# Optimization experiments

Hardware: AMD Instinct MI355X
Metric: run time of the kernel (lower is better)

The kernel has to match this reference:

```python
import jax, jax.numpy as jnp
import numpy as np

B, N, D, H = 8, 2048, 768, 64

def setup_inputs() -> dict:
    key = jax.random.key(0)
    k1, k2, k3, k4 = jax.random.split(key, 4)
    return {
        "input": jax.random.normal(k1, (B, N, D), dtype=jnp.float32),
        "Wq": jax.random.normal(k2, (D, H), dtype=jnp.float32) * (D ** -0.5),
        "Wk": jax.random.normal(k3, (D, H), dtype=jnp.float32) * (D ** -0.5),
        "Wv": jax.random.normal(k4, (D, H), dtype=jnp.float32) * (D ** -0.5),
    }

def reference(input, Wq, Wk, Wv):
    # Projections: [B, N, H]
    Q = jnp.einsum('bnd,dh->bnh', input, Wq)
    K = jnp.einsum('bnd,dh->bnh', input, Wk)
    V = jnp.einsum('bnd,dh->bnh', input, Wv)
    # Raw scores [B, N, N]; mask BEFORE scaling (as in original; -inf/scale == -inf)
    scores = jnp.einsum('bqh,bkh->bqk', Q, K)
    n = input.shape[1]
    causal = jnp.tril(jnp.ones((n, n), dtype=bool))
    scores = jnp.where(causal, scores, -jnp.inf)
    scores = scores / (K.shape[-1] ** 0.5)
    attn = jax.nn.softmax(scores, axis=-1)
    # dropout_rate=0 -> identity (eval mode)
    return jnp.einsum('bqk,bkh->bqh', attn, V)
```

## Files before the change

### kernel.cpp

```cpp
#include <hip/hip_runtime.h>
#include <stdint.h>

typedef __bf16 bf16_t;
typedef __bf16 bf16x4 __attribute__((ext_vector_type(4)));
typedef __bf16 bf16x8 __attribute__((ext_vector_type(8)));
typedef float floatx4 __attribute__((ext_vector_type(4)));
typedef float floatx16 __attribute__((ext_vector_type(16)));

#define B_ 8
#define N_ 2048
#define D_ 768
#define H_ 64

#define WAIT_VM8()   { __builtin_amdgcn_sched_barrier(0); __builtin_amdgcn_s_waitcnt(0x0F78); __builtin_amdgcn_sched_barrier(0); }
#define WAIT_VM0()   { __builtin_amdgcn_sched_barrier(0); __builtin_amdgcn_s_waitcnt(0x0F70); __builtin_amdgcn_sched_barrier(0); }
#define WAIT_LGKM0() { __builtin_amdgcn_sched_barrier(0); __builtin_amdgcn_s_waitcnt(0xC07F); __builtin_amdgcn_sched_barrier(0); }

__device__ __forceinline__ bf16_t f2bf(float f) {
    union { float f; uint32_t u; } v; v.f = f;
    uint32_t u = v.u;
    uint32_t r = (u + 0x7fffu + ((u >> 16) & 1u)) >> 16;
    union { unsigned short s; bf16_t b; } o; o.s = (unsigned short)r;
    return o.b;
}

__device__ __forceinline__ void async_cp16(void* l, const void* g) {
    __builtin_amdgcn_global_load_lds(
        (const __attribute__((address_space(1))) uint32_t*)g,
        (__attribute__((address_space(3))) uint32_t*)l, 16, 0, 0);
}

__global__ void wt_kernel(const float* __restrict__ Wq,
                          const float* __restrict__ Wk,
                          const float* __restrict__ Wv,
                          bf16_t* __restrict__ Wt) {
    const int h = threadIdx.x;
    const int k = blockIdx.x;
    const int s = blockIdx.y;
    const float* W = (s == 0) ? Wq : (s == 1) ? Wk : Wv;
    float v = W[k * H_ + h];
    if (s == 0) v *= 0.125f * 1.4426950408889634f;
    Wt[(size_t)(s * 64 + h) * D_ + k] = f2bf(v);
}

__launch_bounds__(256, 2)
__global__ void proj_kernel(const float* __restrict__ X,
                            const bf16_t* __restrict__ Wt,
                            bf16_t* __restrict__ Qb,
                            bf16_t* __restrict__ Kb,
                            bf16_t* __restrict__ Vt) {
    const int wave = threadIdx.x >> 6;
    const int lane = threadIdx.x & 63;
    const int quad = lane >> 4;
    const int l16  = lane & 15;
    const int rowhalf = wave & 1;
    const int colhalf = wave >> 1;
    const int m0blk = blockIdx.x * 32;

    __shared__ __align__(16) float  As[2][32 * 64];
    __shared__ __align__(16) bf16_t Bs[2][192 * 64];

    floatx4 acc[6];
#pragma unroll
    for (int i = 0; i < 6; i++) acc[i] = (floatx4){0.f, 0.f, 0.f, 0.f};

    auto stage = [&](int buf, int k0) {
#pragma unroll
        for (int i = 0; i < 2; i++) {
            const int r = (wave * 2 + i) * 4 + (lane >> 4);
            const int c = (lane & 15) ^ (r & 15);
            const float* g = X + (size_t)(m0blk + r) * D_ + k0 + c * 4;
            async_cp16((char*)&As[buf][0] + (wave * 2 + i) * 1024, g);
        }
#pragma unroll
        for (int i = 0; i < 6; i++) {
            const int r = (wave * 6 + i) * 8 + (lane >> 3);
            const int c = (lane & 7) ^ (r & 7);
            const bf16_t* g = Wt + (size_t)r * D_ + k0 + c * 8;
            async_cp16((char*)&Bs[buf][0] + (wave * 6 + i) * 1024, g);
        }
    };

    const int arow = rowhalf * 16 + l16;

    stage(0, 0);
    for (int ch = 0; ch < 12; ch++) {
        __syncthreads();
        if (ch + 1 < 12) stage((ch + 1) & 1, (ch + 1) * 64);

        const char* Ab = (const char*)&As[ch & 1][0];
        const char* Bb = (const char*)&Bs[ch & 1][0];
#pragma unroll
        for (int kh = 0; kh < 2; kh++) {
            const int c0 = kh * 8 + quad * 2;
            float4 xa = *(const float4*)(Ab + arow * 256 + ((c0 ^ l16) & 15) * 16);
            float4 xb = *(const float4*)(Ab + arow * 256 + (((c0 + 1) ^ l16) & 15) * 16);
            bf16x8 af;
            af[0] = f2bf(xa.x); af[1] = f2bf(xa.y);
            af[2] = f2bf(xa.z); af[3] = f2bf(xa.w);
            af[4] = f2bf(xb.x); af[5] = f2bf(xb.y);
            af[6] = f2bf(xb.z); af[7] = f2bf(xb.w);
            const int cb = kh * 4 + quad;
#pragma unroll
            for (int nt = 0; nt < 6; nt++) {
                const int n = colhalf * 96 + nt * 16 + l16;
                bf16x8 bf = *(const bf16x8*)(Bb + n * 128 + ((cb ^ (n & 7))) * 16);
                acc[nt] = __builtin_amdgcn_mfma_f32_16x16x32_bf16(af, bf, acc[nt], 0, 0, 0);
            }
        }
    }

#pragma unroll
    for (int nt = 0; nt < 6; nt++) {
        const int c = colhalf * 96 + nt * 16 + l16;
#pragma unroll
        for (int r = 0; r < 4; r++) {
            const int m = m0blk + rowhalf * 16 + quad * 4 + r;
            bf16_t val = f2bf(acc[nt][r]);
            if (c < 64) {
                Qb[(size_t)m * H_ + c] = val;
            } else if (c < 128) {
                Kb[(size_t)m * H_ + (c - 64)] = val;
            } else {
                const int b = m >> 11, n = m & 2047, h = c - 128;
                Vt[((size_t)b * H_ + h) * N_ + n] = val;
            }
        }
    }
}

__launch_bounds__(256, 2)
__global__ void attn_kernel(const bf16_t* __restrict__ Qb,
                            const bf16_t* __restrict__ Kb,
                            const bf16_t* __restrict__ Vt,
                            float* __restrict__ Out) {
    const int x = blockIdx.x;
    const int b = blockIdx.y;
    const int z = blockIdx.z;
    const int qt = z ? (63 - x) : x;
    const int q0 = qt * 32;

    const int wave = threadIdx.x >> 6;
    const int lane = threadIdx.x & 63;
    const int hi   = lane >> 5;
    const int lq   = lane & 31;

    __shared__ __align__(16) char smem[4 * 16384 + 4 * 2048];
    char* mybase = smem + wave * 16384;
    char* Pimg   = smem + 65536 + wave * 2048;
    float* Ol = (float*)smem;
    float* Ll = (float*)(smem + 24576);

    const bf16_t* qrow = Qb + ((size_t)b * N_ + q0 + lq) * H_ + hi * 8;
    bf16x8 qf0 = *(const bf16x8*)(qrow);
    bf16x8 qf1 = *(const bf16x8*)(qrow + 16);
    bf16x8 qf2 = *(const bf16x8*)(qrow + 32);
    bf16x8 qf3 = *(const bf16x8*)(qrow + 48);

    floatx16 o0, o1;
#pragma unroll
    for (int i = 0; i < 16; i++) { o0[i] = 0.f; o1[i] = 0.f; }
    float ls = 0.f;

    const bf16_t* KpB = Kb + (size_t)b * N_ * H_;
    const bf16_t* VpB = Vt + (size_t)b * H_ * N_;

    const int rK = lane >> 3, cK = lane & 7;
    const int rV = lane >> 2, cV = lane & 3;
    const int mVl = (rV & 3) ^ ((rV & 4) >> 2);
    auto stage_kv = [&](int k0, char* buf) {
#pragma unroll
        for (int i = 0; i < 4; i++) {
            const int r = i * 8 + rK;
            const int mk = rK ^ (((i & 1) << 2));
            async_cp16(buf + i * 1024,
                       KpB + (size_t)(k0 + r) * H_ + (cK ^ mk) * 8);
        }
#pragma unroll
        for (int i = 0; i < 4; i++) {
            const int h = i * 16 + rV;
            async_cp16(buf + 4096 + i * 1024,
                       VpB + (size_t)h * N_ + k0 + (cV ^ mVl) * 8);
        }
    };

    const int ktm = qt;
    if (wave <= ktm)     stage_kv(wave * 32, mybase);
    if (wave + 4 <= ktm) stage_kv((wave + 4) * 32, mybase + 8192);

    const int mK = (lq & 7) ^ ((lq & 8) >> 1);
    const int m8 = (lq & 7) ^ ((lq & 8) >> 1);

    for (int kt = wave; kt <= ktm; kt += 4) {
        const int k0 = kt * 32;
        char* kb = mybase + (((((kt - wave) >> 2) & 1)) ? 8192 : 0);
        char* vb = kb + 4096;

        if (kt + 4 <= ktm) { WAIT_VM8(); } else { WAIT_VM0(); }

        bf16x8 kf0 = *(const bf16x8*)(kb + lq * 128 + (((0 + hi) ^ mK) * 16));
        bf16x8 kf1 = *(const bf16x8*)(kb + lq * 128 + (((2 + hi) ^ mK) * 16));
        bf16x8 kf2 = *(const bf16x8*)(kb + lq * 128 + (((4 + hi) ^ mK) * 16));
        bf16x8 kf3 = *(const bf16x8*)(kb + lq * 128 + (((6 + hi) ^ mK) * 16));
        const int mV0 = (lq & 3) ^ ((lq & 4) >> 2);
        bf16x8 vf00 = *(const bf16x8*)(vb + (lq     ) * 64 + (((0 + hi) ^ mV0) * 16));
        bf16x8 vf01 = *(const bf16x8*)(vb + (lq     ) * 64 + (((2 + hi) ^ mV0) * 16));
        bf16x8 vf10 = *(const bf16x8*)(vb + (lq + 32) * 64 + (((0 + hi) ^ mV0) * 16));
        bf16x8 vf11 = *(const bf16x8*)(vb + (lq + 32) * 64 + (((2 + hi) ^ mV0) * 16));

        WAIT_LGKM0();
        if (kt + 8 <= ktm) stage_kv(k0 + 256, kb);

        floatx16 st;
#pragma unroll
        for (int i = 0; i < 16; i++) st[i] = 0.f;
        st = __builtin_amdgcn_mfma_f32_32x32x16_bf16(kf0, qf0, st, 0, 0, 0);
        st = __builtin_amdgcn_mfma_f32_32x32x16_bf16(kf1, qf1, st, 0, 0, 0);
        st = __builtin_amdgcn_mfma_f32_32x32x16_bf16(kf2, qf2, st, 0, 0, 0);
        st = __builtin_amdgcn_mfma_f32_32x32x16_bf16(kf3, qf3, st, 0, 0, 0);

        float p[16];
        if (kt < qt) {
#pragma unroll
            for (int r = 0; r < 16; r++) p[r] = exp2f(st[r]);
        } else {
#pragma unroll
            for (int r = 0; r < 16; r++) {
                const int row = (r & 3) + 8 * (r >> 2) + 4 * hi;
                p[r] = (row <= lq) ? exp2f(st[r]) : 0.f;
            }
        }
#pragma unroll
        for (int r = 0; r < 16; r++) ls += p[r];

#pragma unroll
        for (int g = 0; g < 4; g++) {
            bf16x4 w;
            w[0] = f2bf(p[g * 4 + 0]); w[1] = f2bf(p[g * 4 + 1]);
            w[2] = f2bf(p[g * 4 + 2]); w[3] = f2bf(p[g * 4 + 3]);
            const int sub = g * 2 + hi;
            *(bf16x4*)(Pimg + lq * 64 + ((sub ^ m8) * 8)) = w;
        }

#pragma unroll
        for (int s2 = 0; s2 < 2; s2++) {
            const int sub0 = s2 * 4 + hi * 2;
            bf16x4 a0 = *(const bf16x4*)(Pimg + lq * 64 + (((sub0    ) ^ m8) * 8));
            bf16x4 a1 = *(const bf16x4*)(Pimg + lq * 64 + (((sub0 + 1) ^ m8) * 8));
            bf16x8 pf;
            pf[0] = a0[0]; pf[1] = a0[1]; pf[2] = a0[2]; pf[3] = a0[3];
            pf[4] = a1[0]; pf[5] = a1[1]; pf[6] = a1[2]; pf[7] = a1[3];
            o0 = __builtin_amdgcn_mfma_f32_32x32x16_bf16(pf, (s2 ? vf01 : vf00), o0, 0, 0, 0);
            o1 = __builtin_amdgcn_mfma_f32_32x32x16_bf16(pf, (s2 ? vf11 : vf10), o1, 0, 0, 0);
        }
    }

    float lst = ls + __shfl_xor(ls, 32, 64);
    __syncthreads();
    if (hi == 0) Ll[wave * 32 + lq] = lst;
    if (wave != 0) {
        float* Ow = Ol + (wave - 1) * 2048;
#pragma unroll
        for (int r = 0; r < 16; r++) {
            const int q = (r & 3) + 8 * (r >> 2) + 4 * hi;
            Ow[q * 64 + lq]      = o0[r];
            Ow[q * 64 + 32 + lq] = o1[r];
        }
    }
    __syncthreads();
    if (wave == 0) {
#pragma unroll
        for (int r = 0; r < 16; r++) {
            const int q = (r & 3) + 8 * (r >> 2) + 4 * hi;
            const float l4 = Ll[q] + Ll[32 + q] + Ll[64 + q] + Ll[96 + q];
            const float inv = 1.0f / l4;
            float v0 = o0[r] + Ol[q * 64 + lq]
                     + Ol[2048 + q * 64 + lq] + Ol[4096 + q * 64 + lq];
            float v1 = o1[r] + Ol[q * 64 + 32 + lq]
                     + Ol[2048 + q * 64 + 32 + lq] + Ol[4096 + q * 64 + 32 + lq];
            const size_t base = ((size_t)b * N_ + q0 + q) * H_;
            Out[base + lq]      = v0 * inv;
            Out[base + 32 + lq] = v1 * inv;
        }
    }
}

extern "C" void kernel_launch(void* const* d_in, const int* in_sizes, int n_in,
                              void* d_out, int out_size, void* d_ws, size_t ws_size,
                              hipStream_t stream) {
    const float* X  = (const float*)d_in[0];
    const float* Wq = (const float*)d_in[1];
    const float* Wk = (const float*)d_in[2];
    const float* Wv = (const float*)d_in[3];
    float* Out = (float*)d_out;

    char* ws = (char*)d_ws;
    bf16_t* Qb = (bf16_t*)(ws);
    bf16_t* Kb = (bf16_t*)(ws + (size_t)(2u << 20));
    bf16_t* Vt = (bf16_t*)(ws + (size_t)(4u << 20));
    bf16_t* Wt = (bf16_t*)(ws + (size_t)(6u << 20));

    hipLaunchKernelGGL(wt_kernel, dim3(768, 3), dim3(64), 0, stream, Wq, Wk, Wv, Wt);
    hipLaunchKernelGGL(proj_kernel, dim3(512), dim3(256), 0, stream, X, Wt, Qb, Kb, Vt);
    hipLaunchKernelGGL(attn_kernel, dim3(32, 8, 2), dim3(256), 0, stream, Qb, Kb, Vt, Out);
}
```

Measured before the change: 120.9 us.

## Split projection columns across blocks and widen attention to eight waves

The projection kernel now splits the 192 output columns across two blocks, which doubles the grid and halves per-block LDS and accumulators. The attention kernel moves to 512 threads with eight waves splitting the key tiles. V is loaded straight from global memory instead of being staged in LDS. The P matrix is repacked into MFMA operand layout with cross-lane shuffles rather than an LDS round trip, and the final reduction is spread over all threads with vectorized stores. These changes aim for more parallelism and less LDS traffic, at the cost of re-reading X twice and issuing uncoalesced, latency-exposed global V loads in the inner loop.

```diff
diff --git a/kernel.cpp b/kernel.cpp
--- a/kernel.cpp
+++ b/kernel.cpp
@@ -2,7 +2,6 @@
 #include <stdint.h>
 
 typedef __bf16 bf16_t;
-typedef __bf16 bf16x4 __attribute__((ext_vector_type(4)));
 typedef __bf16 bf16x8 __attribute__((ext_vector_type(8)));
 typedef float floatx4 __attribute__((ext_vector_type(4)));
 typedef float floatx16 __attribute__((ext_vector_type(16)));
@@ -12,7 +11,6 @@
 #define D_ 768
 #define H_ 64
 
-#define WAIT_VM8()   { __builtin_amdgcn_sched_barrier(0); __builtin_amdgcn_s_waitcnt(0x0F78); __builtin_amdgcn_sched_barrier(0); }
 #define WAIT_VM0()   { __builtin_amdgcn_sched_barrier(0); __builtin_amdgcn_s_waitcnt(0x0F70); __builtin_amdgcn_sched_barrier(0); }
 #define WAIT_LGKM0() { __builtin_amdgcn_sched_barrier(0); __builtin_amdgcn_s_waitcnt(0xC07F); __builtin_amdgcn_sched_barrier(0); }
 
@@ -22,6 +20,12 @@
     uint32_t r = (u + 0x7fffu + ((u >> 16) & 1u)) >> 16;
     union { unsigned short s; bf16_t b; } o; o.s = (unsigned short)r;
     return o.b;
+}
+
+__device__ __forceinline__ uint32_t pkbf(float lo, float hi_) {
+    union { bf16_t b[2]; uint32_t u; } t;
+    t.b[0] = f2bf(lo); t.b[1] = f2bf(hi_);
+    return t.u;
 }
 
 __device__ __forceinline__ void async_cp16(void* l, const void* g) {
@@ -43,7 +47,7 @@
     Wt[(size_t)(s * 64 + h) * D_ + k] = f2bf(v);
 }
 
-__launch_bounds__(256, 2)
+__launch_bounds__(256, 4)
 __global__ void proj_kernel(const float* __restrict__ X,
                             const bf16_t* __restrict__ Wt,
                             bf16_t* __restrict__ Qb,
@@ -55,14 +59,16 @@
     const int l16  = lane & 15;
     const int rowhalf = wave & 1;
     const int colhalf = wave >> 1;
-    const int m0blk = blockIdx.x * 32;
+    const int nb = blockIdx.x & 1;
+    const int colbase = nb * 96;
+    const int m0blk = (blockIdx.x >> 1) * 32;
 
     __shared__ __align__(16) float  As[2][32 * 64];
-    __shared__ __align__(16) bf16_t Bs[2][192 * 64];
-
-    floatx4 acc[6];
-#pragma unroll
-    for (int i = 0; i < 6; i++) acc[i] = (floatx4){0.f, 0.f, 0.f, 0.f};
+    __shared__ __align__(16) bf16_t Bs[2][96 * 64];
+
+    floatx4 acc[3];
+#pragma unroll
+    for (int i = 0; i < 3; i++) acc[i] = (floatx4){0.f, 0.f, 0.f, 0.f};
 
     auto stage = [&](int buf, int k0) {
 #pragma unroll
@@ -73,11 +79,11 @@
             async_cp16((char*)&As[buf][0] + (wave * 2 + i) * 1024, g);
         }
 #pragma unroll
-        for (int i = 0; i < 6; i++) {
-            const int r = (wave * 6 + i) * 8 + (lane >> 3);
+        for (int i = 0; i < 3; i++) {
+            const int r = (wave * 3 + i) * 8 + (lane >> 3);
             const int c = (lane & 7) ^ (r & 7);
-            const bf16_t* g = Wt + (size_t)r * D_ + k0 + c * 8;
-            async_cp16((char*)&Bs[buf][0] + (wave * 6 + i) * 1024, g);
+            const bf16_t* g = Wt + (size_t)(colbase + r) * D_ + k0 + c * 8;
+            async_cp16((char*)&Bs[buf][0] + (wave * 3 + i) * 1024, g);
         }
     };
 
@@ -102,17 +108,17 @@
             af[6] = f2bf(xb.z); af[7] = f2bf(xb.w);
             const int cb = kh * 4 + quad;
 #pragma unroll
-            for (int nt = 0; nt < 6; nt++) {
-                const int n = colhalf * 96 + nt * 16 + l16;
-                bf16x8 bf = *(const bf16x8*)(Bb + n * 128 + ((cb ^ (n & 7))) * 16);
+            for (int nt = 0; nt < 3; nt++) {
+                const int nl = colhalf * 48 + nt * 16 + l16;
+                bf16x8 bf = *(const bf16x8*)(Bb + nl * 128 + ((cb ^ (nl & 7))) * 16);
                 acc[nt] = __builtin_amdgcn_mfma_f32_16x16x32_bf16(af, bf, acc[nt], 0, 0, 0);
             }
         }
     }
 
 #pragma unroll
-    for (int nt = 0; nt < 6; nt++) {
-        const int c = colhalf * 96 + nt * 16 + l16;
+    for (int nt = 0; nt < 3; nt++) {
+        const int c = colbase + colhalf * 48 + nt * 16 + l16;
 #pragma unroll
         for (int r = 0; r < 4; r++) {
             const int m = m0blk + rowhalf * 16 + quad * 4 + r;
@@ -129,7 +135,7 @@
     }
 }
 
-__launch_bounds__(256, 2)
+__launch_bounds__(512, 4)
 __global__ void attn_kernel(const bf16_t* __restrict__ Qb,
                             const bf16_t* __restrict__ Kb,
                             const bf16_t* __restrict__ Vt,
@@ -140,16 +146,19 @@
     const int qt = z ? (63 - x) : x;
     const int q0 = qt * 32;
 
-    const int wave = threadIdx.x >> 6;
-    const int lane = threadIdx.x & 63;
+    const int tid  = threadIdx.x;
+    const int wave = tid >> 6;
+    const int lane = tid & 63;
     const int hi   = lane >> 5;
     const int lq   = lane & 31;
 
-    __shared__ __align__(16) char smem[4 * 16384 + 4 * 2048];
-    char* mybase = smem + wave * 16384;
-    char* Pimg   = smem + 65536 + wave * 2048;
+    __shared__ __align__(16) char smem[8 * 8192 + 1024];
+    char* mybase = smem + wave * 8192;
     float* Ol = (float*)smem;
-    float* Ll = (float*)(smem + 24576);
+    float* Ll = (float*)(smem + 65536);
+
+    const bf16_t* KpB = Kb + (size_t)b * N_ * H_;
+    const bf16_t* VpB = Vt + (size_t)b * H_ * N_;
 
     const bf16_t* qrow = Qb + ((size_t)b * N_ + q0 + lq) * H_ + hi * 8;
     bf16x8 qf0 = *(const bf16x8*)(qrow);
@@ -162,54 +171,43 @@
     for (int i = 0; i < 16; i++) { o0[i] = 0.f; o1[i] = 0.f; }
     float ls = 0.f;
 
-    const bf16_t* KpB = Kb + (size_t)b * N_ * H_;
-    const bf16_t* VpB = Vt + (size_t)b * H_ * N_;
-
     const int rK = lane >> 3, cK = lane & 7;
-    const int rV = lane >> 2, cV = lane & 3;
-    const int mVl = (rV & 3) ^ ((rV & 4) >> 2);
-    auto stage_kv = [&](int k0, char* buf) {
+    auto stage_k = [&](int k0, char* buf) {
 #pragma unroll
         for (int i = 0; i < 4; i++) {
             const int r = i * 8 + rK;
-            const int mk = rK ^ (((i & 1) << 2));
+            const int mk = rK ^ ((i & 1) << 2);
             async_cp16(buf + i * 1024,
                        KpB + (size_t)(k0 + r) * H_ + (cK ^ mk) * 8);
         }
-#pragma unroll
-        for (int i = 0; i < 4; i++) {
-            const int h = i * 16 + rV;
-            async_cp16(buf + 4096 + i * 1024,
-                       VpB + (size_t)h * N_ + k0 + (cV ^ mVl) * 8);
-        }
     };
 
     const int ktm = qt;
-    if (wave <= ktm)     stage_kv(wave * 32, mybase);
-    if (wave + 4 <= ktm) stage_kv((wave + 4) * 32, mybase + 8192);
+    if (wave <= ktm)     stage_k(wave * 32, mybase);
+    if (wave + 8 <= ktm) stage_k((wave + 8) * 32, mybase + 4096);
 
     const int mK = (lq & 7) ^ ((lq & 8) >> 1);
-    const int m8 = (lq & 7) ^ ((lq & 8) >> 1);
-
-    for (int kt = wave; kt <= ktm; kt += 4) {
+
+    for (int kt = wave; kt <= ktm; kt += 8) {
         const int k0 = kt * 32;
-        char* kb = mybase + (((((kt - wave) >> 2) & 1)) ? 8192 : 0);
-        char* vb = kb + 4096;
-
-        if (kt + 4 <= ktm) { WAIT_VM8(); } else { WAIT_VM0(); }
+        char* kb = mybase + (((kt - wave) >> 3) & 1) * 4096;
+
+        if (kt == wave) { WAIT_VM0(); }
 
         bf16x8 kf0 = *(const bf16x8*)(kb + lq * 128 + (((0 + hi) ^ mK) * 16));
         bf16x8 kf1 = *(const bf16x8*)(kb + lq * 128 + (((2 + hi) ^ mK) * 16));
         bf16x8 kf2 = *(const bf16x8*)(kb + lq * 128 + (((4 + hi) ^ mK) * 16));
         bf16x8 kf3 = *(const bf16x8*)(kb + lq * 128 + (((6 + hi) ^ mK) * 16));
-        const int mV0 = (lq & 3) ^ ((lq & 4) >> 2);
-        bf16x8 vf00 = *(const bf16x8*)(vb + (lq     ) * 64 + (((0 + hi) ^ mV0) * 16));
-        bf16x8 vf01 = *(const bf16x8*)(vb + (lq     ) * 64 + (((2 + hi) ^ mV0) * 16));
-        bf16x8 vf10 = *(const bf16x8*)(vb + (lq + 32) * 64 + (((0 + hi) ^ mV0) * 16));
-        bf16x8 vf11 = *(const bf16x8*)(vb + (lq + 32) * 64 + (((2 + hi) ^ mV0) * 16));
-
         WAIT_LGKM0();
-        if (kt + 8 <= ktm) stage_kv(k0 + 256, kb);
+
+        const bf16_t* vrow0 = VpB + (size_t)lq * N_ + k0 + 8 * hi;
+        const bf16_t* vrow1 = vrow0 + (size_t)32 * N_;
+        bf16x8 vf00 = *(const bf16x8*)(vrow0);
+        bf16x8 vf01 = *(const bf16x8*)(vrow0 + 16);
+        bf16x8 vf10 = *(const bf16x8*)(vrow1);
+        bf16x8 vf11 = *(const bf16x8*)(vrow1 + 16);
+        __builtin_amdgcn_sched_barrier(0);
+        if (kt + 16 <= ktm) stage_k(k0 + 512, kb);
 
         floatx16 st;
 #pragma unroll
@@ -219,69 +217,65 @@
         st = __builtin_amdgcn_mfma_f32_32x32x16_bf16(kf2, qf2, st, 0, 0, 0);
         st = __builtin_amdgcn_mfma_f32_32x32x16_bf16(kf3, qf3, st, 0, 0, 0);
 
-        float p[16];
         if (kt < qt) {
 #pragma unroll
-            for (int r = 0; r < 16; r++) p[r] = exp2f(st[r]);
+            for (int r = 0; r < 16; r++) st[r] = exp2f(st[r]);
         } else {
 #pragma unroll
             for (int r = 0; r < 16; r++) {
                 const int row = (r & 3) + 8 * (r >> 2) + 4 * hi;
-                p[r] = (row <= lq) ? exp2f(st[r]) : 0.f;
+                st[r] = (row <= lq) ? exp2f(st[r]) : 0.f;
             }
         }
 #pragma unroll
-        for (int r = 0; r < 16; r++) ls += p[r];
-
-#pragma unroll
-        for (int g = 0; g < 4; g++) {
-            bf16x4 w;
-            w[0] = f2bf(p[g * 4 + 0]); w[1] = f2bf(p[g * 4 + 1]);
-            w[2] = f2bf(p[g * 4 + 2]); w[3] = f2bf(p[g * 4 + 3]);
-            const int sub = g * 2 + hi;
-            *(bf16x4*)(Pimg + lq * 64 + ((sub ^ m8) * 8)) = w;
-        }
-
-#pragma unroll
-        for (int s2 = 0; s2 < 2; s2++) {
-            const int sub0 = s2 * 4 + hi * 2;
-            bf16x4 a0 = *(const bf16x4*)(Pimg + lq * 64 + (((sub0    ) ^ m8) * 8));
-            bf16x4 a1 = *(const bf16x4*)(Pimg + lq * 64 + (((sub0 + 1) ^ m8) * 8));
-            bf16x8 pf;
-            pf[0] = a0[0]; pf[1] = a0[1]; pf[2] = a0[2]; pf[3] = a0[3];
-            pf[4] = a1[0]; pf[5] = a1[1]; pf[6] = a1[2]; pf[7] = a1[3];
-            o0 = __builtin_amdgcn_mfma_f32_32x32x16_bf16(pf, (s2 ? vf01 : vf00), o0, 0, 0, 0);
-            o1 = __builtin_amdgcn_mfma_f32_32x32x16_bf16(pf, (s2 ? vf11 : vf10), o1, 0, 0, 0);
-        }
+        for (int r = 0; r < 16; r++) ls += st[r];
+
+        uint32_t pb[8];
+#pragma unroll
+        for (int t = 0; t < 8; t++) pb[t] = pkbf(st[2 * t], st[2 * t + 1]);
+        uint32_t rc[4];
+#pragma unroll
+        for (int t = 0; t < 4; t++) {
+            const uint32_t w = hi ? pb[(t & 1) + 4 * (t >> 1)]
+                                  : pb[(t & 1) + 2 + 4 * (t >> 1)];
+            rc[t] = (uint32_t)__shfl_xor((int)w, 32, 64);
+        }
+        union { uint32_t u[4]; bf16x8 v; } f0, f1;
+        f0.u[0] = hi ? rc[0] : pb[0]; f0.u[1] = hi ? rc[1] : pb[1];
+        f0.u[2] = hi ? pb[2] : rc[0]; f0.u[3] = hi ? pb[3] : rc[1];
+        f1.u[0] = hi ? rc[2] : pb[4]; f1.u[1] = hi ? rc[3] : pb[5];
+        f1.u[2] = hi ? pb[6] : rc[2]; f1.u[3] = hi ? pb[7] : rc[3];
+
+        o0 = __builtin_amdgcn_mfma_f32_32x32x16_bf16(f0.v, vf00, o0, 0, 0, 0);
+        o0 = __builtin_amdgcn_mfma_f32_32x32x16_bf16(f1.v, vf01, o0, 0, 0, 0);
+        o1 = __builtin_amdgcn_mfma_f32_32x32x16_bf16(f0.v, vf10, o1, 0, 0, 0);
+        o1 = __builtin_amdgcn_mfma_f32_32x32x16_bf16(f1.v, vf11, o1, 0, 0, 0);
     }
 
     float lst = ls + __shfl_xor(ls, 32, 64);
     __syncthreads();
     if (hi == 0) Ll[wave * 32 + lq] = lst;
-    if (wave != 0) {
-        float* Ow = Ol + (wave - 1) * 2048;
-#pragma unroll
-        for (int r = 0; r < 16; r++) {
-            const int q = (r & 3) + 8 * (r >> 2) + 4 * hi;
-            Ow[q * 64 + lq]      = o0[r];
-            Ow[q * 64 + 32 + lq] = o1[r];
-        }
+#pragma unroll
+    for (int r = 0; r < 16; r++) {
+        const int q = (r & 3) + 8 * (r >> 2) + 4 * hi;
+        Ol[((size_t)wave * 32 + q) * 64 + lq]      = o0[r];
+        Ol[((size_t)wave * 32 + q) * 64 + 32 + lq] = o1[r];
     }
     __syncthreads();
-    if (wave == 0) {
-#pragma unroll
-        for (int r = 0; r < 16; r++) {
-            const int q = (r & 3) + 8 * (r >> 2) + 4 * hi;
-            const float l4 = Ll[q] + Ll[32 + q] + Ll[64 + q] + Ll[96 + q];
-            const float inv = 1.0f / l4;
-            float v0 = o0[r] + Ol[q * 64 + lq]
-                     + Ol[2048 + q * 64 + lq] + Ol[4096 + q * 64 + lq];
-            float v1 = o1[r] + Ol[q * 64 + 32 + lq]
-                     + Ol[2048 + q * 64 + 32 + lq] + Ol[4096 + q * 64 + 32 + lq];
-            const size_t base = ((size_t)b * N_ + q0 + q) * H_;
-            Out[base + lq]      = v0 * inv;
-            Out[base + 32 + lq] = v1 * inv;
-        }
+    {
+        const int q  = tid >> 4;
+        const int h4 = (tid & 15) * 4;
+        floatx4 a = (floatx4){0.f, 0.f, 0.f, 0.f};
+        float l = 0.f;
+#pragma unroll
+        for (int w = 0; w < 8; w++) {
+            const floatx4 part = *(const floatx4*)&Ol[((size_t)w * 32 + q) * 64 + h4];
+            a += part;
+            l += Ll[w * 32 + q];
+        }
+        const float inv = 1.0f / l;
+        float4 outv = {a[0] * inv, a[1] * inv, a[2] * inv, a[3] * inv};
+        *(float4*)&Out[((size_t)b * N_ + q0 + q) * H_ + h4] = outv;
     }
 }
 
@@ -301,6 +295,6 @@
     bf16_t* Wt = (bf16_t*)(ws + (size_t)(6u << 20));
 
     hipLaunchKernelGGL(wt_kernel, dim3(768, 3), dim3(64), 0, stream, Wq, Wk, Wv, Wt);
-    hipLaunchKernelGGL(proj_kernel, dim3(512), dim3(256), 0, stream, X, Wt, Qb, Kb, Vt);
-    hipLaunchKernelGGL(attn_kernel, dim3(32, 8, 2), dim3(256), 0, stream, Qb, Kb, Vt, Out);
-}
+    hipLaunchKernelGGL(proj_kernel, dim3(1024), dim3(256), 0, stream, X, Wt, Qb, Kb, Vt);
+    hipLaunchKernelGGL(attn_kernel, dim3(32, 8, 2), dim3(512), 0, stream, Qb, Kb, Vt, Out);
+}
```

After: 120.6 us. About the same (-0.3%).
